# Kernel tuning notes

Measured on AMD Instinct MI355X. Metric: run time of the kernel, lower is better.

Reference implementation:

```python
import jax, jax.numpy as jnp
from jax import lax
import numpy as np

THRESHOLD = 1.0
SMOOTH_FACTOR = 1.0
NOISE_THRESHOLD = 0.0
TAIL_THRESHOLD = 0.0


def setup_inputs() -> dict:
    key = jax.random.key(0)
    k1, k2 = jax.random.split(key)
    B, T, D = 16, 1024, 512
    hidden = jax.random.normal(k1, (B, T, D), jnp.float32)
    # scale so sigmoid(h @ w) is not saturated -> realistic fire rate
    w_cif = jax.random.normal(k2, (D,), jnp.float32) * 0.05
    b_cif = jnp.zeros((1,), jnp.float32)
    return {"hidden": hidden, "w_cif": w_cif, "b_cif": b_cif}


def _cif(hidden, alphas, threshold):
    # hidden: [B, T, D], alphas: [B, T]
    B, T, D = hidden.shape

    def step(carry, xs):
        integrate, frame = carry          # [B], [B, D]
        alpha, h_t = xs                   # [B], [B, D]
        dist_completion = 1.0 - integrate
        integrate = integrate + alpha
        fire = integrate >= threshold     # [B] bool
        cur = jnp.where(fire, dist_completion, alpha)
        remainds = alpha - cur
        frame_out = frame + cur[:, None] * h_t
        new_integrate = jnp.where(fire, integrate - 1.0, integrate)
        new_frame = jnp.where(fire[:, None], remainds[:, None] * h_t, frame_out)
        return (new_integrate, new_frame), (integrate, frame_out)

    init = (jnp.zeros((B,), alphas.dtype), jnp.zeros((B, D), hidden.dtype))
    xs = (jnp.swapaxes(alphas, 0, 1), jnp.swapaxes(hidden, 0, 1))  # time-major
    _, (fires, frames) = lax.scan(step, init, xs)
    fires = jnp.swapaxes(fires, 0, 1)    # [B, T]
    frames = jnp.swapaxes(frames, 0, 1)  # [B, T, D]

    # left-pack fired frames per batch (torch slices to max fired count;
    # here we keep the jit-static full length T, extra slots are zero)
    fire_idxs = fires >= threshold
    pos = jnp.cumsum(fire_idxs.astype(jnp.int32), axis=1) - 1
    pos = jnp.where(fire_idxs, pos, T)   # non-fired -> out of range, dropped

    def pack(p, f):
        return jnp.zeros((T, D), f.dtype).at[p].set(f, mode='drop')

    frame_fires = jax.vmap(pack)(pos, frames)  # [B, T, D]
    return frame_fires, fires


def reference(hidden, w_cif, b_cif):
    B, T, D = hidden.shape
    # forward_cnn: Linear(idim,1) -> sigmoid -> relu(smooth*a - noise)
    alphas = jax.nn.sigmoid(hidden @ w_cif + b_cif[0])          # [B, T]
    alphas = jax.nn.relu(alphas * SMOOTH_FACTOR - NOISE_THRESHOLD)
    # tail_process_fn: append a zero step, add tail threshold
    alphas = jnp.concatenate([alphas, jnp.zeros((B, 1), alphas.dtype)], axis=1)
    alphas = alphas + TAIL_THRESHOLD
    hidden = jnp.concatenate([hidden, jnp.zeros((B, 1, D), hidden.dtype)], axis=1)
    token_num = jnp.floor(alphas.sum(-1))
    acoustic_embeds, cif_peak = _cif(hidden, alphas, THRESHOLD)
    return acoustic_embeds, token_num, alphas, cif_peak
```

## Files before the change

kernel.cpp:

```cpp
#include <hip/hip_runtime.h>
#include <math.h>

#define BB 16
#define TT 1024
#define T1 1025
#define DD 512

__device__ __forceinline__ float fract_exact(float x) {
#if defined(__has_builtin)
#if __has_builtin(__builtin_amdgcn_fractf)
    return __builtin_amdgcn_fractf(x);
#else
    return x - floorf(x);
#endif
#else
    return x - floorf(x);
#endif
}

__global__ __launch_bounds__(256) void alpha_kernel(
    const float* __restrict__ hidden,
    const float* __restrict__ w,
    const float* __restrict__ bias,
    float* __restrict__ alphas_out)
{
    int row  = blockIdx.x * 4 + (threadIdx.x >> 6);
    int lane = threadIdx.x & 63;
    const float* h = hidden + (size_t)row * DD;
    float4 x0 = *(const float4*)(h + lane * 4);
    float4 x1 = *(const float4*)(h + 256 + lane * 4);
    float4 w0 = *(const float4*)(w + lane * 4);
    float4 w1 = *(const float4*)(w + 256 + lane * 4);
    float s = x0.x * w0.x + x0.y * w0.y + x0.z * w0.z + x0.w * w0.w
            + x1.x * w1.x + x1.y * w1.y + x1.z * w1.z + x1.w * w1.w;
    #pragma unroll
    for (int off = 32; off > 0; off >>= 1) s += __shfl_down(s, off, 64);
    if (lane == 0) {
        float x = s + bias[0];
        float sig = 1.0f / (1.0f + expf(-x));
        int b = row >> 10;
        int t = row & 1023;
        alphas_out[b * T1 + t] = sig;
    }
}

__global__ __launch_bounds__(128) void scan_kernel(
    float* __restrict__ alphas_out,
    float* __restrict__ token_num,
    float* __restrict__ cif_peak,
    int*   __restrict__ fire_time,
    int*   __restrict__ nfired)
{
    int b   = blockIdx.x;
    int tid = threadIdx.x;

    __shared__ float a_sh[TT + 128];
    __shared__ float peak_sh[T1 + 3];

    for (int t = tid; t < TT; t += 128) a_sh[t] = alphas_out[b * T1 + t];
    for (int t = TT + tid; t < TT + 128; t += 128) a_sh[t] = 0.0f;
    __syncthreads();

    if (tid == 0) {
        const float4* a4 = (const float4*)a_sh;
        float4* p4 = (float4*)peak_sh;
        float integrate = 0.0f;

        float4 buf[4][8];
        #pragma unroll
        for (int k = 0; k < 8; ++k) {
            buf[0][k] = a4[k];
            buf[1][k] = a4[8 + k];
            buf[2][k] = a4[16 + k];
            buf[3][k] = a4[24 + k];
        }

        #pragma unroll 4
        for (int c = 0; c < 32; ++c) {
            float4 P[8];
            #pragma unroll
            for (int k = 0; k < 8; ++k) {
                float4 A = buf[c & 3][k];
                float n0 = integrate + A.x; P[k].x = n0; float i0 = fract_exact(n0);
                float n1 = i0 + A.y;        P[k].y = n1; float i1 = fract_exact(n1);
                float n2 = i1 + A.z;        P[k].z = n2; float i2 = fract_exact(n2);
                float n3 = i2 + A.w;        P[k].w = n3; integrate = fract_exact(n3);
            }
            #pragma unroll
            for (int k = 0; k < 8; ++k) p4[c * 8 + k] = P[k];
            #pragma unroll
            for (int k = 0; k < 8; ++k) buf[c & 3][k] = a4[(c + 4) * 8 + k];
        }
        peak_sh[TT] = integrate;
    } else if (tid >= 64) {
        int lane = tid - 64;
        double s = 0.0;
        for (int t = lane; t < TT; t += 64) s += (double)a_sh[t];
        #pragma unroll
        for (int off = 32; off > 0; off >>= 1) s += __shfl_down(s, off, 64);
        if (lane == 0) {
            token_num[b] = (float)floor(s);
            alphas_out[b * T1 + TT] = 0.0f;
        }
    }
    __syncthreads();

    for (int t = tid; t < T1; t += 128) cif_peak[b * T1 + t] = peak_sh[t];

    if (tid < 64) {
        int cnt = 0;
        int* ft_b = fire_time + b * T1;
        for (int base = 0; base < T1; base += 64) {
            int t = base + tid;
            bool f = (t < T1) && (peak_sh[t] >= 1.0f);
            unsigned long long m = __ballot(f);
            int pos = cnt + __popcll(m & ((1ull << tid) - 1ull));
            if (f) ft_b[pos] = t;
            cnt += __popcll(m);
        }
        if (tid == 0) nfired[b] = cnt;
    }
}

__global__ __launch_bounds__(128) void fill_kernel(
    const float* __restrict__ hidden,
    const float* __restrict__ alphas,
    const float* __restrict__ peak,
    const int*   __restrict__ fire_time,
    const int*   __restrict__ nfired,
    float* __restrict__ ae)
{
    int idx = blockIdx.x;
    int b = idx / T1;
    int j = idx % T1;
    int d = threadIdx.x * 4;
    float4* out4 = (float4*)(ae + ((size_t)b * T1 + j) * DD + d);

    int nf = nfired[b];
    if (j >= nf) {
        *out4 = make_float4(0.f, 0.f, 0.f, 0.f);
        return;
    }
    const int*   ft_b = fire_time + b * T1;
    const float* a_b  = alphas + b * T1;
    const float* pk_b = peak + b * T1;
    const float* hb   = hidden + (size_t)b * TT * DD + d;

    int e = ft_b[j];
    float4 acc = make_float4(0.f, 0.f, 0.f, 0.f);
    int t0;
    if (j > 0) {
        int s = ft_b[j - 1];
        float ps   = (s > 0) ? pk_b[s - 1] : 0.0f;
        float ips  = (ps >= 1.0f) ? ps - 1.0f : ps;
        float curs = 1.0f - ips;
        float r    = a_b[s] - curs;
        float4 h = *(const float4*)(hb + (size_t)s * DD);
        acc.x = r * h.x; acc.y = r * h.y; acc.z = r * h.z; acc.w = r * h.w;
        t0 = s + 1;
    } else {
        t0 = 0;
    }
    for (int t = t0; t < e; ++t) {
        float c = a_b[t];
        float4 h = *(const float4*)(hb + (size_t)t * DD);
        acc.x += c * h.x; acc.y += c * h.y; acc.z += c * h.z; acc.w += c * h.w;
    }
    {
        float pe  = (e > 0) ? pk_b[e - 1] : 0.0f;
        float ipe = (pe >= 1.0f) ? pe - 1.0f : pe;
        float ce  = 1.0f - ipe;
        float4 h = *(const float4*)(hb + (size_t)e * DD);
        acc.x += ce * h.x; acc.y += ce * h.y; acc.z += ce * h.z; acc.w += ce * h.w;
    }
    *out4 = acc;
}

extern "C" void kernel_launch(void* const* d_in, const int* in_sizes, int n_in,
                              void* d_out, int out_size, void* d_ws, size_t ws_size,
                              hipStream_t stream) {
    const float* hidden = (const float*)d_in[0];
    const float* w      = (const float*)d_in[1];
    const float* bias   = (const float*)d_in[2];

    float* out        = (float*)d_out;
    float* ae         = out;
    float* token_num  = out + (size_t)BB * T1 * DD;
    float* alphas_out = token_num + BB;
    float* cif_peak   = alphas_out + (size_t)BB * T1;

    int* fire_time = (int*)d_ws;
    int* nfired    = fire_time + (size_t)BB * T1;

    alpha_kernel<<<(BB * TT) / 4, 256, 0, stream>>>(hidden, w, bias, alphas_out);
    scan_kernel<<<BB, 128, 0, stream>>>(alphas_out, token_num, cif_peak,
                                        fire_time, nfired);
    fill_kernel<<<BB * T1, 128, 0, stream>>>(hidden, alphas_out, cif_peak,
                                             fire_time, nfired, ae);
}
```

Baseline: 39.28 us.

## Run CIF scan for all batches in one workgroup, one lane per batch

Replaces the 16-block scan kernel with a single 256-thread block. Sixteen lanes of the first wavefront each run the serial fire-integration scan for one batch, reading alphas and writing peaks directly in global memory instead of staging them through LDS. The other wavefronts compute token counts, and after a barrier each wavefront compacts fire indices for four batches. This drops the LDS staging and the per-block copy-out. In exchange, the scan reads global memory with an 8-deep prefetch and uses unaligned float4 accesses on odd batch rows, so it may stall on L2 latency, and the compaction step is now serialised across batches.

```diff
diff --git a/kernel.cpp b/kernel.cpp
--- a/kernel.cpp
+++ b/kernel.cpp
@@ -44,81 +44,68 @@
     }
 }
 
-__global__ __launch_bounds__(128) void scan_kernel(
+__global__ __launch_bounds__(256) void scan_kernel(
     float* __restrict__ alphas_out,
     float* __restrict__ token_num,
     float* __restrict__ cif_peak,
     int*   __restrict__ fire_time,
     int*   __restrict__ nfired)
 {
-    int b   = blockIdx.x;
-    int tid = threadIdx.x;
+    int tid  = threadIdx.x;
+    int wv   = tid >> 6;
+    int lane = tid & 63;
 
-    __shared__ float a_sh[TT + 128];
-    __shared__ float peak_sh[T1 + 3];
+    if (wv == 0) {
+        if (lane < 16) {
+            int b = lane;
+            const float* a_b  = alphas_out + b * T1;
+            float*       pk_b = cif_peak   + b * T1;
 
-    for (int t = tid; t < TT; t += 128) a_sh[t] = alphas_out[b * T1 + t];
-    for (int t = TT + tid; t < TT + 128; t += 128) a_sh[t] = 0.0f;
-    __syncthreads();
+            float4 buf[8];
+            #pragma unroll
+            for (int k = 0; k < 8; ++k) buf[k] = *(const float4*)(a_b + 4 * k);
 
-    if (tid == 0) {
-        const float4* a4 = (const float4*)a_sh;
-        float4* p4 = (float4*)peak_sh;
-        float integrate = 0.0f;
-
-        float4 buf[4][8];
-        #pragma unroll
-        for (int k = 0; k < 8; ++k) {
-            buf[0][k] = a4[k];
-            buf[1][k] = a4[8 + k];
-            buf[2][k] = a4[16 + k];
-            buf[3][k] = a4[24 + k];
+            float integrate = 0.0f;
+            #pragma unroll 8
+            for (int i = 0; i < 256; ++i) {
+                float4 A = buf[i & 7];
+                if (i < 248)
+                    buf[i & 7] = *(const float4*)(a_b + 4 * i + 32);
+                float4 P;
+                float n0 = integrate + A.x; P.x = n0; float i0 = fract_exact(n0);
+                float n1 = i0 + A.y;        P.y = n1; float i1 = fract_exact(n1);
+                float n2 = i1 + A.z;        P.z = n2; float i2 = fract_exact(n2);
+                float n3 = i2 + A.w;        P.w = n3; integrate = fract_exact(n3);
+                *(float4*)(pk_b + 4 * i) = P;
+            }
+            pk_b[TT] = integrate;
         }
-
-        #pragma unroll 4
-        for (int c = 0; c < 32; ++c) {
-            float4 P[8];
+    } else {
+        for (int b = wv - 1; b < BB; b += 3) {
+            const float* a_b = alphas_out + b * T1;
+            double s = 0.0;
+            for (int t = lane; t < TT; t += 64) s += (double)a_b[t];
             #pragma unroll
-            for (int k = 0; k < 8; ++k) {
-                float4 A = buf[c & 3][k];
-                float n0 = integrate + A.x; P[k].x = n0; float i0 = fract_exact(n0);
-                float n1 = i0 + A.y;        P[k].y = n1; float i1 = fract_exact(n1);
-                float n2 = i1 + A.z;        P[k].z = n2; float i2 = fract_exact(n2);
-                float n3 = i2 + A.w;        P[k].w = n3; integrate = fract_exact(n3);
-            }
-            #pragma unroll
-            for (int k = 0; k < 8; ++k) p4[c * 8 + k] = P[k];
-            #pragma unroll
-            for (int k = 0; k < 8; ++k) buf[c & 3][k] = a4[(c + 4) * 8 + k];
+            for (int off = 32; off > 0; off >>= 1) s += __shfl_down(s, off, 64);
+            if (lane == 0) token_num[b] = (float)floor(s);
         }
-        peak_sh[TT] = integrate;
-    } else if (tid >= 64) {
-        int lane = tid - 64;
-        double s = 0.0;
-        for (int t = lane; t < TT; t += 64) s += (double)a_sh[t];
-        #pragma unroll
-        for (int off = 32; off > 0; off >>= 1) s += __shfl_down(s, off, 64);
-        if (lane == 0) {
-            token_num[b] = (float)floor(s);
-            alphas_out[b * T1 + TT] = 0.0f;
-        }
+        if (wv == 1 && lane < BB) alphas_out[lane * T1 + TT] = 0.0f;
     }
     __syncthreads();
 
-    for (int t = tid; t < T1; t += 128) cif_peak[b * T1 + t] = peak_sh[t];
-
-    if (tid < 64) {
+    for (int b = wv * 4; b < wv * 4 + 4; ++b) {
+        const float* pk_b = cif_peak + b * T1;
+        int* ft_b = fire_time + b * T1;
         int cnt = 0;
-        int* ft_b = fire_time + b * T1;
         for (int base = 0; base < T1; base += 64) {
-            int t = base + tid;
-            bool f = (t < T1) && (peak_sh[t] >= 1.0f);
+            int t = base + lane;
+            bool f = (t < T1) && (pk_b[t] >= 1.0f);
             unsigned long long m = __ballot(f);
-            int pos = cnt + __popcll(m & ((1ull << tid) - 1ull));
+            int pos = cnt + __popcll(m & ((1ull << lane) - 1ull));
             if (f) ft_b[pos] = t;
             cnt += __popcll(m);
         }
-        if (tid == 0) nfired[b] = cnt;
+        if (lane == 0) nfired[b] = cnt;
     }
 }
 
@@ -193,8 +180,8 @@
     int* nfired    = fire_time + (size_t)BB * T1;
 
     alpha_kernel<<<(BB * TT) / 4, 256, 0, stream>>>(hidden, w, bias, alphas_out);
-    scan_kernel<<<BB, 128, 0, stream>>>(alphas_out, token_num, cif_peak,
-                                        fire_time, nfired);
+    scan_kernel<<<1, 256, 0, stream>>>(alphas_out, token_num, cif_peak,
+                                       fire_time, nfired);
     fill_kernel<<<BB * T1, 128, 0, stream>>>(hidden, alphas_out, cif_peak,
                                              fire_time, nfired, ae);
 }
```

New measurement: 66.39 us. +69.0%, slower.
